# Optimization experiments

Measured on AMD Instinct MI355X. Metric: run time of the kernel, lower is better.

Reference implementation:

```python
import jax, jax.numpy as jnp
import numpy as np

B, C, H, W = 4, 256, 64, 64


def setup_inputs() -> dict:
    key = jax.random.key(0)
    ks = jax.random.split(key, 8)
    s = 0.02
    return {
        "x": jax.random.normal(ks[0], (B, C, H, W), dtype=jnp.float32),
        "Wq": jax.random.normal(ks[1], (C, C), dtype=jnp.float32) * s,
        "bq": jax.random.normal(ks[2], (C,), dtype=jnp.float32) * s,
        "Wk": jax.random.normal(ks[3], (C, C), dtype=jnp.float32) * s,
        "bk": jax.random.normal(ks[4], (C,), dtype=jnp.float32) * s,
        "Wv": jax.random.normal(ks[5], (C, C), dtype=jnp.float32) * s,
        "bv": jax.random.normal(ks[6], (C,), dtype=jnp.float32) * s,
        "gamma": jax.random.normal(ks[7], (1,), dtype=jnp.float32),
    }


def reference(x, Wq, bq, Wk, bk, Wv, bv, gamma):
    b, c, h, w = x.shape
    n = h * w
    xf = x.reshape(b, c, n)  # [B,C,N]
    # 1x1 convs == per-pixel linear over channels
    q = jnp.einsum("oc,bcn->bon", Wq, xf) + bq[None, :, None]  # [B,C,N]
    k = jnp.einsum("oc,bcn->bon", Wk, xf) + bk[None, :, None]  # [B,C,N]
    v = jnp.einsum("oc,bcn->bon", Wv, xf) + bv[None, :, None]  # [B,C,N]
    # energy[b,i,j] = sum_c q[b,c,i] * k[b,c,j]  (Q^T K, no scale in original)
    energy = jnp.einsum("bci,bcj->bij", q, k)  # [B,N,N]
    attention = jax.nn.softmax(energy, axis=-1)  # softmax over j
    # out = V @ attention^T : out[b,c,i] = sum_j v[b,c,j] * attention[b,i,j]
    out = jnp.einsum("bcj,bij->bci", v, attention)  # [B,C,N]
    out = gamma[0] * out + xf
    return out.reshape(b, c, h, w)
```

## Files before the change

kernel.cpp:

```cpp
#include <hip/hip_runtime.h>
#include <hip/hip_bf16.h>

#define Bb 4
#define Cc 256
#define Nn 4096
#define NV 4160

typedef short s16x8 __attribute__((ext_vector_type(8)));
typedef float f32x4 __attribute__((ext_vector_type(4)));

__device__ __forceinline__ unsigned short f2bf(float f) {
    unsigned u = __builtin_bit_cast(unsigned, f);
    u += 0x7FFFu + ((u >> 16) & 1u);
    return (unsigned short)(u >> 16);
}

__device__ __forceinline__ f32x4 mfma16(s16x8 a, s16x8 b, f32x4 c) {
    return __builtin_amdgcn_mfma_f32_16x16x32_bf16(a, b, c, 0, 0, 0);
}

#if __has_builtin(__builtin_amdgcn_global_load_lds)
#define GL16(g, sdst)                                                              \
    __builtin_amdgcn_global_load_lds(                                              \
        (const __attribute__((address_space(1))) unsigned int*)(g),                \
        (__attribute__((address_space(3))) unsigned int*)(sdst), 16, 0, 0)
#else
#define GL16(g, sdst)                                                              \
    do {                                                                           \
        *(s16x8*)((char*)(sdst) + (threadIdx.x & 63) * 16) = *(const s16x8*)(g);   \
    } while (0)
#endif

__global__ void prep_w(const float* __restrict__ Wq, const float* __restrict__ Wk,
                       const float* __restrict__ Wv, unsigned short* __restrict__ Wbf) {
    int idx = (blockIdx.x * 256 + threadIdx.x) * 8;
    int mat = idx >> 16;
    int off = idx & 65535;
    const float* src = (mat == 0) ? Wq : ((mat == 1) ? Wk : Wv);
    float4 a = *(const float4*)(src + off);
    float4 b = *(const float4*)(src + off + 4);
    s16x8 o;
    o[0] = (short)f2bf(a.x); o[1] = (short)f2bf(a.y);
    o[2] = (short)f2bf(a.z); o[3] = (short)f2bf(a.w);
    o[4] = (short)f2bf(b.x); o[5] = (short)f2bf(b.y);
    o[6] = (short)f2bf(b.z); o[7] = (short)f2bf(b.w);
    *(s16x8*)(Wbf + idx) = o;
}

__global__ void transpose_x(const float* __restrict__ x, unsigned short* __restrict__ xT) {
    int b = blockIdx.z, c0 = blockIdx.y * 64, n0 = blockIdx.x * 64;
    __shared__ float tile[64][65];
    int t = threadIdx.x;
    int r = t >> 2, q = t & 3;
    const float* src = x + ((size_t)(b * Cc + c0 + r)) * Nn + n0 + q * 16;
#pragma unroll
    for (int j = 0; j < 4; j++) {
        float4 v4 = *(const float4*)(src + j * 4);
        tile[r][q * 16 + j * 4 + 0] = v4.x;
        tile[r][q * 16 + j * 4 + 1] = v4.y;
        tile[r][q * 16 + j * 4 + 2] = v4.z;
        tile[r][q * 16 + j * 4 + 3] = v4.w;
    }
    __syncthreads();
    unsigned short* dst = xT + ((size_t)b * Nn + n0 + r) * Cc + c0 + q * 16;
    s16x8 o0, o1;
#pragma unroll
    for (int j = 0; j < 8; j++) o0[j] = (short)f2bf(tile[q * 16 + j][r]);
#pragma unroll
    for (int j = 0; j < 8; j++) o1[j] = (short)f2bf(tile[q * 16 + 8 + j][r]);
    *(s16x8*)dst = o0;
    *(s16x8*)(dst + 8) = o1;
}

__global__ void proj(const unsigned short* __restrict__ xT, const unsigned short* __restrict__ Wbf,
                     const float* __restrict__ bq, const float* __restrict__ bk,
                     const float* __restrict__ bv,
                     unsigned short* __restrict__ qT, unsigned short* __restrict__ kT,
                     unsigned short* __restrict__ vO) {
    int nt0 = blockIdx.x * 64;
    int mat = blockIdx.y;
    int b   = blockIdx.z;
    int t = threadIdx.x, w = t >> 6, l = t & 63;
    int lr = l & 15, lg = l >> 4;
    const unsigned short* Wm  = Wbf + mat * (Cc * Cc);
    const float* bias = (mat == 0) ? bq : ((mat == 1) ? bk : bv);
    const unsigned short* xTb = xT + (size_t)b * Nn * Cc;

    if (mat < 2) {
        unsigned short* out = ((mat == 0) ? qT : kT) + (size_t)b * Nn * Cc;
        int nrow = nt0 + w * 16;
        s16x8 af[8];
#pragma unroll
        for (int kk = 0; kk < 8; kk++)
            af[kk] = *(const s16x8*)(xTb + (nrow + lr) * Cc + kk * 32 + lg * 8);
        for (int ct = 0; ct < 16; ct++) {
            f32x4 acca = {0, 0, 0, 0}, accb = {0, 0, 0, 0};
#pragma unroll
            for (int kk = 0; kk < 8; kk += 2) {
                s16x8 bfa = *(const s16x8*)(Wm + (ct * 16 + lr) * Cc + kk * 32 + lg * 8);
                s16x8 bfb = *(const s16x8*)(Wm + (ct * 16 + lr) * Cc + (kk + 1) * 32 + lg * 8);
                acca = mfma16(af[kk], bfa, acca);
                accb = mfma16(af[kk + 1], bfb, accb);
            }
            f32x4 acc = acca + accb;
            float bb = bias[ct * 16 + lr];
#pragma unroll
            for (int r = 0; r < 4; r++)
                out[(nrow + lg * 4 + r) * Cc + ct * 16 + lr] = f2bf(acc[r] + bb);
        }
    } else {
        unsigned short* out = vO + (size_t)b * Cc * NV;
        for (int mt = 0; mt < 4; mt++) {
            int crow = (w * 4 + mt) * 16;
            s16x8 af[8];
#pragma unroll
            for (int kk = 0; kk < 8; kk++)
                af[kk] = *(const s16x8*)(Wm + (crow + lr) * Cc + kk * 32 + lg * 8);
#pragma unroll
            for (int nt = 0; nt < 4; nt++) {
                f32x4 acca = {0, 0, 0, 0}, accb = {0, 0, 0, 0};
#pragma unroll
                for (int kk = 0; kk < 8; kk += 2) {
                    s16x8 bfa = *(const s16x8*)(xTb + (nt0 + nt * 16 + lr) * Cc + kk * 32 + lg * 8);
                    s16x8 bfb = *(const s16x8*)(xTb + (nt0 + nt * 16 + lr) * Cc + (kk + 1) * 32 + lg * 8);
                    acca = mfma16(af[kk], bfa, acca);
                    accb = mfma16(af[kk + 1], bfb, accb);
                }
                f32x4 acc = acca + accb;
#pragma unroll
                for (int r = 0; r < 4; r++) {
                    float bb = bias[crow + lg * 4 + r];
                    out[(size_t)(crow + lg * 4 + r) * NV + nt0 + nt * 16 + lr] = f2bf(acc[r] + bb);
                }
            }
        }
    }
}

__global__ void __launch_bounds__(256, 2)
attn(const unsigned short* __restrict__ qT, const unsigned short* __restrict__ kT,
     const unsigned short* __restrict__ vv,
     float* __restrict__ OPT, float* __restrict__ lp) {
    int id = blockIdx.x;
    int bs = id & 7, b = bs >> 1, s = bs & 1, iblk = id >> 3;
    int t = threadIdx.x, w = t >> 6, l = t & 63;
    int lr = l & 15, lg = l >> 4;
    int i0 = iblk * 64 + w * 16;

    __shared__ char Ks[2][16384];
    __shared__ char Vs[2][16384];
    __shared__ unsigned short P_lds[4][512];
    unsigned short* pl = P_lds[w];

    const unsigned short* qb = qT + ((size_t)b * Nn + i0) * Cc;
    const char* kbase = (const char*)(kT + ((size_t)b * Nn + s * 2048) * Cc);
    const char* vbase = (const char*)(vv + (size_t)b * Cc * NV + s * 2048);

    s16x8 qf[8];
#pragma unroll
    for (int kk = 0; kk < 8; kk++)
        qf[kk] = *(const s16x8*)(qb + lr * Cc + kk * 32 + lg * 8);

    f32x4 O[16];
#pragma unroll
    for (int ct = 0; ct < 16; ct++) O[ct] = {0, 0, 0, 0};
    float lsum[4] = {0, 0, 0, 0};
    const float L2E = 1.44269504088896340736f;

#define STAGEK(bufi, jt)                                                        \
    {                                                                           \
        const char* ksl_ = kbase + (size_t)(jt) * 16384;                        \
        _Pragma("unroll") for (int i_ = 0; i_ < 4; i_++) {                      \
            int chunk_ = w * 4 + i_;                                            \
            int L_ = chunk_ * 1024 + l * 16;                                    \
            int row_ = L_ >> 9;                                                 \
            GL16(ksl_ + (L_ ^ ((row_ & 7) << 4)), &Ks[bufi][chunk_ * 1024]);    \
        }                                                                       \
    }

#define STAGEV(bufi, jt)                                                        \
    {                                                                           \
        _Pragma("unroll") for (int i_ = 0; i_ < 4; i_++) {                      \
            int chunk_ = w * 4 + i_;                                            \
            int row_ = chunk_ * 16 + (l >> 2);                                  \
            int colb_ = ((l & 3) * 16) ^ (((l >> 3) & 3) << 4);                 \
            GL16(vbase + (size_t)row_ * (NV * 2) + (size_t)(jt) * 64 + colb_,   \
                 &Vs[bufi][chunk_ * 1024]);                                     \
        }                                                                       \
    }

    STAGEK(0, 0);
    STAGEV(0, 0);
    asm volatile("s_waitcnt vmcnt(0)" ::: "memory");
    __syncthreads();
    int buf = 0;

    for (int jt = 0; jt < 64; jt++) {
        if (jt < 63) {
            STAGEK(buf ^ 1, jt + 1);
            STAGEV(buf ^ 1, jt + 1);
        }
        const char* ksb = Ks[buf];
        f32x4 E0 = {0, 0, 0, 0}, E1 = {0, 0, 0, 0};
#pragma unroll
        for (int kk = 0; kk < 8; kk++) {
            int cb = (kk * 64 + lg * 16) ^ ((lr & 7) << 4);
            s16x8 k0 = *(const s16x8*)(ksb + lr * 512 + cb);
            s16x8 k1 = *(const s16x8*)(ksb + (16 + lr) * 512 + cb);
            E0 = mfma16(qf[kk], k0, E0);
            E1 = mfma16(qf[kk], k1, E1);
        }
        float p0[4], p1[4];
#pragma unroll
        for (int r = 0; r < 4; r++) {
            p0[r] = exp2f(E0[r] * L2E);
            p1[r] = exp2f(E1[r] * L2E);
            lsum[r] += p0[r] + p1[r];
        }
#pragma unroll
        for (int r = 0; r < 4; r++) {
            pl[(lg * 4 + r) * 32 + lr] = f2bf(p0[r]);
            pl[(lg * 4 + r) * 32 + 16 + lr] = f2bf(p1[r]);
        }
        const char* vsb = Vs[buf];
        int vswz = (lg * 16) ^ (((lr >> 1) & 3) << 4);
        s16x8 vfr[16];
#pragma unroll
        for (int ct = 0; ct < 16; ct++)
            vfr[ct] = *(const s16x8*)(vsb + (ct * 16 + lr) * 64 + vswz);
        asm volatile("s_waitcnt lgkmcnt(0)" ::: "memory");
        __builtin_amdgcn_sched_barrier(0);
        s16x8 pf = *(const s16x8*)(pl + lr * 32 + lg * 8);
#pragma unroll
        for (int ct = 0; ct < 16; ct++)
            O[ct] = mfma16(pf, vfr[ct], O[ct]);
        asm volatile("s_waitcnt vmcnt(0)" ::: "memory");
        __syncthreads();
        buf ^= 1;
    }

#pragma unroll
    for (int r = 0; r < 4; r++) {
#pragma unroll
        for (int msk = 1; msk <= 8; msk <<= 1)
            lsum[r] += __shfl_xor(lsum[r], msk);
    }
    size_t sb = (size_t)(s * Bb + b);
    if (lr == 0) {
#pragma unroll
        for (int r = 0; r < 4; r++)
            lp[sb * Nn + i0 + lg * 4 + r] = lsum[r];
    }
    float* ob = OPT + sb * Nn * Cc;
#pragma unroll
    for (int ct = 0; ct < 16; ct++) {
#pragma unroll
        for (int r = 0; r < 4; r++)
            ob[(size_t)(i0 + lg * 4 + r) * Cc + ct * 16 + lr] = O[ct][r];
    }
#undef STAGEK
#undef STAGEV
}

__global__ void __launch_bounds__(256)
merge(const float* __restrict__ OPT, const float* __restrict__ lp,
      const float* __restrict__ x, const float* __restrict__ gamma,
      float* __restrict__ out) {
    int b = blockIdx.z, c0 = blockIdx.y * 64, n0 = blockIdx.x * 64;
    __shared__ float tile[64][65];
    __shared__ float linv[64];
    int t = threadIdx.x;
    if (t < 64) {
        float sum = lp[(size_t)b * Nn + n0 + t] + lp[(size_t)(Bb + b) * Nn + n0 + t];
        linv[t] = 1.0f / sum;
    }
    __syncthreads();
    float g = gamma[0];
    int r = t >> 2, q = t & 3;
    const float* p0 = OPT + ((size_t)b * Nn + n0 + r) * Cc + c0 + q * 16;
    const float* p1 = OPT + ((size_t)(Bb + b) * Nn + n0 + r) * Cc + c0 + q * 16;
    float sc = g * linv[r];
#pragma unroll
    for (int j = 0; j < 4; j++) {
        float4 a0 = *(const float4*)(p0 + j * 4);
        float4 a1 = *(const float4*)(p1 + j * 4);
        tile[r][q * 16 + j * 4 + 0] = sc * (a0.x + a1.x);
        tile[r][q * 16 + j * 4 + 1] = sc * (a0.y + a1.y);
        tile[r][q * 16 + j * 4 + 2] = sc * (a0.z + a1.z);
        tile[r][q * 16 + j * 4 + 3] = sc * (a0.w + a1.w);
    }
    __syncthreads();
    const float* xp = x + ((size_t)b * Cc + c0 + r) * Nn + n0 + q * 16;
    float* op = out + ((size_t)b * Cc + c0 + r) * Nn + n0 + q * 16;
#pragma unroll
    for (int j = 0; j < 4; j++) {
        float4 xv = *(const float4*)(xp + j * 4);
        float4 o4;
        o4.x = tile[q * 16 + j * 4 + 0][r] + xv.x;
        o4.y = tile[q * 16 + j * 4 + 1][r] + xv.y;
        o4.z = tile[q * 16 + j * 4 + 2][r] + xv.z;
        o4.w = tile[q * 16 + j * 4 + 3][r] + xv.w;
        *(float4*)(op + j * 4) = o4;
    }
}

extern "C" void kernel_launch(void* const* d_in, const int* in_sizes, int n_in,
                              void* d_out, int out_size, void* d_ws, size_t ws_size,
                              hipStream_t stream) {
    (void)in_sizes; (void)n_in; (void)out_size; (void)ws_size;
    const float* x     = (const float*)d_in[0];
    const float* Wq    = (const float*)d_in[1];
    const float* bq    = (const float*)d_in[2];
    const float* Wk    = (const float*)d_in[3];
    const float* bk    = (const float*)d_in[4];
    const float* Wv    = (const float*)d_in[5];
    const float* bv    = (const float*)d_in[6];
    const float* gamma = (const float*)d_in[7];
    float* out = (float*)d_out;

    const size_t XTN = (size_t)Bb * Nn * Cc;
    const size_t VSZ = (size_t)Bb * Cc * NV;
    unsigned short* xT  = (unsigned short*)d_ws;
    unsigned short* Wbf = xT + XTN;
    unsigned short* qT  = Wbf + 3 * Cc * Cc;
    unsigned short* kT  = qT + XTN;
    unsigned short* vv  = kT + XTN;
    float*          OPT = (float*)(vv + VSZ);
    float*          lp  = OPT + 2 * XTN;

    hipLaunchKernelGGL(prep_w, dim3(96), dim3(256), 0, stream, Wq, Wk, Wv, Wbf);
    hipLaunchKernelGGL(transpose_x, dim3(Nn / 64, Cc / 64, Bb), dim3(256), 0, stream, x, xT);
    hipLaunchKernelGGL(proj, dim3(Nn / 64, 3, Bb), dim3(256), 0, stream,
                       xT, Wbf, bq, bk, bv, qT, kT, vv);
    hipLaunchKernelGGL(attn, dim3(512), dim3(256), 0, stream,
                       qT, kT, vv, OPT, lp);
    hipLaunchKernelGGL(merge, dim3(Nn / 64, Cc / 64, Bb), dim3(256), 0, stream,
                       OPT, lp, x, gamma, out);
}
```

Measured before the change: 180.1 us.

## Transpose MFMA operands and shuffle P in registers instead of LDS round-trip

```diff
diff --git a/kernel.cpp b/kernel.cpp
--- a/kernel.cpp
+++ b/kernel.cpp
@@ -13,6 +13,10 @@
     unsigned u = __builtin_bit_cast(unsigned, f);
     u += 0x7FFFu + ((u >> 16) & 1u);
     return (unsigned short)(u >> 16);
+}
+
+__device__ __forceinline__ unsigned pk2bf(float a, float b) {
+    return (unsigned)f2bf(a) | ((unsigned)f2bf(b) << 16);
 }
 
 __device__ __forceinline__ f32x4 mfma16(s16x8 a, s16x8 b, f32x4 c) {
@@ -149,8 +153,6 @@
 
     __shared__ char Ks[2][16384];
     __shared__ char Vs[2][16384];
-    __shared__ unsigned short P_lds[4][512];
-    unsigned short* pl = P_lds[w];
 
     const unsigned short* qb = qT + ((size_t)b * Nn + i0) * Cc;
     const char* kbase = (const char*)(kT + ((size_t)b * Nn + s * 2048) * Cc);
@@ -164,7 +166,7 @@
     f32x4 O[16];
 #pragma unroll
     for (int ct = 0; ct < 16; ct++) O[ct] = {0, 0, 0, 0};
-    float lsum[4] = {0, 0, 0, 0};
+    float lsum = 0.f;
     const float L2E = 1.44269504088896340736f;
 
 #define STAGEK(bufi, jt)                                                        \
@@ -202,62 +204,67 @@
         }
         const char* ksb = Ks[buf];
         f32x4 E0 = {0, 0, 0, 0}, E1 = {0, 0, 0, 0};
+        __builtin_amdgcn_s_setprio(1);
 #pragma unroll
         for (int kk = 0; kk < 8; kk++) {
             int cb = (kk * 64 + lg * 16) ^ ((lr & 7) << 4);
             s16x8 k0 = *(const s16x8*)(ksb + lr * 512 + cb);
             s16x8 k1 = *(const s16x8*)(ksb + (16 + lr) * 512 + cb);
-            E0 = mfma16(qf[kk], k0, E0);
-            E1 = mfma16(qf[kk], k1, E1);
-        }
+            E0 = mfma16(k0, qf[kk], E0);
+            E1 = mfma16(k1, qf[kk], E1);
+        }
+        __builtin_amdgcn_s_setprio(0);
+        const char* vsb = Vs[buf];
+        int vswz = (lg * 16) ^ (((lr >> 1) & 3) << 4);
+        s16x8 vfr[16];
+#pragma unroll
+        for (int ct = 0; ct < 16; ct++)
+            vfr[ct] = *(const s16x8*)(vsb + (ct * 16 + lr) * 64 + vswz);
         float p0[4], p1[4];
 #pragma unroll
         for (int r = 0; r < 4; r++) {
             p0[r] = exp2f(E0[r] * L2E);
             p1[r] = exp2f(E1[r] * L2E);
-            lsum[r] += p0[r] + p1[r];
-        }
-#pragma unroll
-        for (int r = 0; r < 4; r++) {
-            pl[(lg * 4 + r) * 32 + lr] = f2bf(p0[r]);
-            pl[(lg * 4 + r) * 32 + 16 + lr] = f2bf(p1[r]);
-        }
-        const char* vsb = Vs[buf];
-        int vswz = (lg * 16) ^ (((lr >> 1) & 3) << 4);
-        s16x8 vfr[16];
+            lsum += p0[r] + p1[r];
+        }
+        unsigned h0a = pk2bf(p0[0], p0[1]), h0b = pk2bf(p0[2], p0[3]);
+        unsigned h1a = pk2bf(p1[0], p1[1]), h1b = pk2bf(p1[2], p1[3]);
+        int sA = lr + ((lg & 1) << 5);
+        int sB = sA + 16;
+        unsigned a0 = (unsigned)__shfl((int)h0a, sA);
+        unsigned b0 = (unsigned)__shfl((int)h1a, sA);
+        unsigned a1 = (unsigned)__shfl((int)h0b, sA);
+        unsigned b1 = (unsigned)__shfl((int)h1b, sA);
+        unsigned a2 = (unsigned)__shfl((int)h0a, sB);
+        unsigned b2 = (unsigned)__shfl((int)h1a, sB);
+        unsigned a3 = (unsigned)__shfl((int)h0b, sB);
+        unsigned b3 = (unsigned)__shfl((int)h1b, sB);
+        bool losel = (lg < 2);
+        uint4 pw;
+        pw.x = losel ? a0 : b0;
+        pw.y = losel ? a1 : b1;
+        pw.z = losel ? a2 : b2;
+        pw.w = losel ? a3 : b3;
+        s16x8 pf = __builtin_bit_cast(s16x8, pw);
+        __builtin_amdgcn_s_setprio(1);
 #pragma unroll
         for (int ct = 0; ct < 16; ct++)
-            vfr[ct] = *(const s16x8*)(vsb + (ct * 16 + lr) * 64 + vswz);
-        asm volatile("s_waitcnt lgkmcnt(0)" ::: "memory");
-        __builtin_amdgcn_sched_barrier(0);
-        s16x8 pf = *(const s16x8*)(pl + lr * 32 + lg * 8);
-#pragma unroll
-        for (int ct = 0; ct < 16; ct++)
-            O[ct] = mfma16(pf, vfr[ct], O[ct]);
+            O[ct] = mfma16(vfr[ct], pf, O[ct]);
+        __builtin_amdgcn_s_setprio(0);
         asm volatile("s_waitcnt vmcnt(0)" ::: "memory");
         __syncthreads();
         buf ^= 1;
     }
 
-#pragma unroll
-    for (int r = 0; r < 4; r++) {
-#pragma unroll
-        for (int msk = 1; msk <= 8; msk <<= 1)
-            lsum[r] += __shfl_xor(lsum[r], msk);
-    }
+    lsum += __shfl_xor(lsum, 16);
+    lsum += __shfl_xor(lsum, 32);
     size_t sb = (size_t)(s * Bb + b);
-    if (lr == 0) {
-#pragma unroll
-        for (int r = 0; r < 4; r++)
-            lp[sb * Nn + i0 + lg * 4 + r] = lsum[r];
-    }
+    if (lg == 0)
+        lp[sb * Nn + i0 + lr] = lsum;
     float* ob = OPT + sb * Nn * Cc;
 #pragma unroll
-    for (int ct = 0; ct < 16; ct++) {
-#pragma unroll
-        for (int r = 0; r < 4; r++)
-            ob[(size_t)(i0 + lg * 4 + r) * Cc + ct * 16 + lr] = O[ct][r];
-    }
+    for (int ct = 0; ct < 16; ct++)
+        *(f32x4*)(ob + (size_t)(i0 + lr) * Cc + ct * 16 + lg * 4) = O[ct];
 #undef STAGEK
 #undef STAGEV
 }
```

Result: slower. 186.5 us (+3.5%).

## Use 32x32 MFMA in attention with register P, 4-way key split, bf16 partials

Applied to the files above, without the earlier changes.

```diff
diff --git a/kernel.cpp b/kernel.cpp
--- a/kernel.cpp
+++ b/kernel.cpp
@@ -8,15 +8,26 @@
 
 typedef short s16x8 __attribute__((ext_vector_type(8)));
 typedef float f32x4 __attribute__((ext_vector_type(4)));
+typedef float f32x16 __attribute__((ext_vector_type(16)));
 
 __device__ __forceinline__ unsigned short f2bf(float f) {
     unsigned u = __builtin_bit_cast(unsigned, f);
     u += 0x7FFFu + ((u >> 16) & 1u);
     return (unsigned short)(u >> 16);
 }
+__device__ __forceinline__ float bf2f(unsigned short u) {
+    unsigned v = ((unsigned)u) << 16;
+    return __builtin_bit_cast(float, v);
+}
+__device__ __forceinline__ unsigned pk2bf(float a, float b) {
+    return (unsigned)f2bf(a) | ((unsigned)f2bf(b) << 16);
+}
 
 __device__ __forceinline__ f32x4 mfma16(s16x8 a, s16x8 b, f32x4 c) {
     return __builtin_amdgcn_mfma_f32_16x16x32_bf16(a, b, c, 0, 0, 0);
+}
+__device__ __forceinline__ f32x16 mfma32(s16x8 a, s16x8 b, f32x16 c) {
+    return __builtin_amdgcn_mfma_f32_32x32x16_bf16(a, b, c, 0, 0, 0);
 }
 
 #if __has_builtin(__builtin_amdgcn_global_load_lds)
@@ -140,31 +151,34 @@
 __global__ void __launch_bounds__(256, 2)
 attn(const unsigned short* __restrict__ qT, const unsigned short* __restrict__ kT,
      const unsigned short* __restrict__ vv,
-     float* __restrict__ OPT, float* __restrict__ lp) {
+     unsigned short* __restrict__ OPT, float* __restrict__ lp) {
     int id = blockIdx.x;
-    int bs = id & 7, b = bs >> 1, s = bs & 1, iblk = id >> 3;
+    int xcd = id & 7, k = id >> 3;
+    int combo = xcd * 2 + (k & 1);
+    int b = combo >> 2, s = combo & 3;
+    int iblk = k >> 1;
     int t = threadIdx.x, w = t >> 6, l = t & 63;
-    int lr = l & 15, lg = l >> 4;
-    int i0 = iblk * 64 + w * 16;
+    int la = l & 31, lh = l >> 5;
+    int i0 = iblk * 128 + w * 32;
 
     __shared__ char Ks[2][16384];
     __shared__ char Vs[2][16384];
-    __shared__ unsigned short P_lds[4][512];
-    unsigned short* pl = P_lds[w];
 
     const unsigned short* qb = qT + ((size_t)b * Nn + i0) * Cc;
-    const char* kbase = (const char*)(kT + ((size_t)b * Nn + s * 2048) * Cc);
-    const char* vbase = (const char*)(vv + (size_t)b * Cc * NV + s * 2048);
-
-    s16x8 qf[8];
-#pragma unroll
-    for (int kk = 0; kk < 8; kk++)
-        qf[kk] = *(const s16x8*)(qb + lr * Cc + kk * 32 + lg * 8);
-
-    f32x4 O[16];
-#pragma unroll
-    for (int ct = 0; ct < 16; ct++) O[ct] = {0, 0, 0, 0};
-    float lsum[4] = {0, 0, 0, 0};
+    const char* kbase = (const char*)(kT + ((size_t)b * Nn + s * 1024) * Cc);
+    const char* vbase = (const char*)(vv + (size_t)b * Cc * NV + s * 1024);
+
+    s16x8 qf[16];
+#pragma unroll
+    for (int kk = 0; kk < 16; kk++)
+        qf[kk] = *(const s16x8*)(qb + la * Cc + kk * 16 + lh * 8);
+
+    f32x16 O[8];
+#pragma unroll
+    for (int ct = 0; ct < 8; ct++)
+#pragma unroll
+        for (int r = 0; r < 16; r++) O[ct][r] = 0.f;
+    float lsum = 0.f;
     const float L2E = 1.44269504088896340736f;
 
 #define STAGEK(bufi, jt)                                                        \
@@ -195,112 +209,129 @@
     __syncthreads();
     int buf = 0;
 
-    for (int jt = 0; jt < 64; jt++) {
-        if (jt < 63) {
+    for (int jt = 0; jt < 32; jt++) {
+        if (jt < 31) {
             STAGEK(buf ^ 1, jt + 1);
             STAGEV(buf ^ 1, jt + 1);
         }
         const char* ksb = Ks[buf];
-        f32x4 E0 = {0, 0, 0, 0}, E1 = {0, 0, 0, 0};
-#pragma unroll
-        for (int kk = 0; kk < 8; kk++) {
-            int cb = (kk * 64 + lg * 16) ^ ((lr & 7) << 4);
-            s16x8 k0 = *(const s16x8*)(ksb + lr * 512 + cb);
-            s16x8 k1 = *(const s16x8*)(ksb + (16 + lr) * 512 + cb);
-            E0 = mfma16(qf[kk], k0, E0);
-            E1 = mfma16(qf[kk], k1, E1);
-        }
-        float p0[4], p1[4];
-#pragma unroll
-        for (int r = 0; r < 4; r++) {
-            p0[r] = exp2f(E0[r] * L2E);
-            p1[r] = exp2f(E1[r] * L2E);
-            lsum[r] += p0[r] + p1[r];
-        }
-#pragma unroll
-        for (int r = 0; r < 4; r++) {
-            pl[(lg * 4 + r) * 32 + lr] = f2bf(p0[r]);
-            pl[(lg * 4 + r) * 32 + 16 + lr] = f2bf(p1[r]);
-        }
+        f32x16 E;
+#pragma unroll
+        for (int r = 0; r < 16; r++) E[r] = 0.f;
+        __builtin_amdgcn_s_setprio(1);
+#pragma unroll
+        for (int kk = 0; kk < 16; kk++) {
+            s16x8 kf = *(const s16x8*)(ksb + la * 512 +
+                                       ((kk * 32 + lh * 16) ^ ((l & 7) << 4)));
+            E = mfma32(kf, qf[kk], E);
+        }
+        __builtin_amdgcn_s_setprio(0);
+#pragma unroll
+        for (int r = 0; r < 16; r++) {
+            float pv = exp2f(E[r] * L2E);
+            E[r] = pv;
+            lsum += pv;
+        }
+        unsigned pk0 = pk2bf(E[0], E[1]),   pk1 = pk2bf(E[2], E[3]);
+        unsigned pk2 = pk2bf(E[4], E[5]),   pk3 = pk2bf(E[6], E[7]);
+        unsigned pk4 = pk2bf(E[8], E[9]),   pk5 = pk2bf(E[10], E[11]);
+        unsigned pk6 = pk2bf(E[12], E[13]), pk7 = pk2bf(E[14], E[15]);
+        unsigned x0 = (unsigned)__shfl_xor((int)pk0, 32);
+        unsigned x1 = (unsigned)__shfl_xor((int)pk1, 32);
+        unsigned x2 = (unsigned)__shfl_xor((int)pk2, 32);
+        unsigned x3 = (unsigned)__shfl_xor((int)pk3, 32);
+        unsigned x4 = (unsigned)__shfl_xor((int)pk4, 32);
+        unsigned x5 = (unsigned)__shfl_xor((int)pk5, 32);
+        unsigned x6 = (unsigned)__shfl_xor((int)pk6, 32);
+        unsigned x7 = (unsigned)__shfl_xor((int)pk7, 32);
+        bool h1 = (lh == 1);
+        uint4 w0, w1;
+        w0.x = h1 ? x2 : pk0;  w0.y = h1 ? x3 : pk1;
+        w0.z = h1 ? pk2 : x0;  w0.w = h1 ? pk3 : x1;
+        w1.x = h1 ? x6 : pk4;  w1.y = h1 ? x7 : pk5;
+        w1.z = h1 ? pk6 : x4;  w1.w = h1 ? pk7 : x5;
+        s16x8 pf0 = __builtin_bit_cast(s16x8, w0);
+        s16x8 pf1 = __builtin_bit_cast(s16x8, w1);
         const char* vsb = Vs[buf];
-        int vswz = (lg * 16) ^ (((lr >> 1) & 3) << 4);
-        s16x8 vfr[16];
-#pragma unroll
-        for (int ct = 0; ct < 16; ct++)
-            vfr[ct] = *(const s16x8*)(vsb + (ct * 16 + lr) * 64 + vswz);
-        asm volatile("s_waitcnt lgkmcnt(0)" ::: "memory");
-        __builtin_amdgcn_sched_barrier(0);
-        s16x8 pf = *(const s16x8*)(pl + lr * 32 + lg * 8);
-#pragma unroll
-        for (int ct = 0; ct < 16; ct++)
-            O[ct] = mfma16(pf, vfr[ct], O[ct]);
+        int vsw = ((l >> 1) & 3) << 4;
+        __builtin_amdgcn_s_setprio(1);
+#pragma unroll
+        for (int ct = 0; ct < 8; ct++) {
+            s16x8 va = *(const s16x8*)(vsb + (ct * 32 + la) * 64 +
+                                       ((lh * 16) ^ vsw));
+            O[ct] = mfma32(va, pf0, O[ct]);
+            s16x8 vb = *(const s16x8*)(vsb + (ct * 32 + la) * 64 +
+                                       ((32 + lh * 16) ^ vsw));
+            O[ct] = mfma32(vb, pf1, O[ct]);
+        }
+        __builtin_amdgcn_s_setprio(0);
         asm volatile("s_waitcnt vmcnt(0)" ::: "memory");
         __syncthreads();
         buf ^= 1;
     }
 
-#pragma unroll
-    for (int r = 0; r < 4; r++) {
-#pragma unroll
-        for (int msk = 1; msk <= 8; msk <<= 1)
-            lsum[r] += __shfl_xor(lsum[r], msk);
-    }
-    size_t sb = (size_t)(s * Bb + b);
-    if (lr == 0) {
-#pragma unroll
-        for (int r = 0; r < 4; r++)
-            lp[sb * Nn + i0 + lg * 4 + r] = lsum[r];
-    }
-    float* ob = OPT + sb * Nn * Cc;
-#pragma unroll
-    for (int ct = 0; ct < 16; ct++) {
-#pragma unroll
-        for (int r = 0; r < 4; r++)
-            ob[(size_t)(i0 + lg * 4 + r) * Cc + ct * 16 + lr] = O[ct][r];
+    lsum += __shfl_xor(lsum, 32);
+    if (l < 32)
+        lp[(size_t)combo * Nn + i0 + l] = lsum;
+    unsigned short* ob = OPT + (size_t)combo * Cc * Nn;
+#pragma unroll
+    for (int ct = 0; ct < 8; ct++) {
+#pragma unroll
+        for (int g = 0; g < 4; g++) {
+#pragma unroll
+            for (int r = 0; r < 4; r++) {
+                int c = ct * 32 + 8 * g + 4 * lh + r;
+                ob[(size_t)c * Nn + i0 + la] = f2bf(O[ct][4 * g + r]);
+            }
+        }
     }
 #undef STAGEK
 #undef STAGEV
 }
 
 __global__ void __launch_bounds__(256)
-merge(const float* __restrict__ OPT, const float* __restrict__ lp,
+merge(const unsigned short* __restrict__ OPT, const float* __restrict__ lp,
       const float* __restrict__ x, const float* __restrict__ gamma,
       float* __restrict__ out) {
     int b = blockIdx.z, c0 = blockIdx.y * 64, n0 = blockIdx.x * 64;
-    __shared__ float tile[64][65];
     __shared__ float linv[64];
     int t = threadIdx.x;
     if (t < 64) {
-        float sum = lp[(size_t)b * Nn + n0 + t] + lp[(size_t)(Bb + b) * Nn + n0 + t];
+        float sum = 0.f;
+#pragma unroll
+        for (int si = 0; si < 4; si++)
+            sum += lp[(size_t)(b * 4 + si) * Nn + n0 + t];
         linv[t] = 1.0f / sum;
     }
     __syncthreads();
     float g = gamma[0];
     int r = t >> 2, q = t & 3;
-    const float* p0 = OPT + ((size_t)b * Nn + n0 + r) * Cc + c0 + q * 16;
-    const float* p1 = OPT + ((size_t)(Bb + b) * Nn + n0 + r) * Cc + c0 + q * 16;
-    float sc = g * linv[r];
-#pragma unroll
-    for (int j = 0; j < 4; j++) {
-        float4 a0 = *(const float4*)(p0 + j * 4);
-        float4 a1 = *(const float4*)(p1 + j * 4);
-        tile[r][q * 16 + j * 4 + 0] = sc * (a0.x + a1.x);
-        tile[r][q * 16 + j * 4 + 1] = sc * (a0.y + a1.y);
-        tile[r][q * 16 + j * 4 + 2] = sc * (a0.z + a1.z);
-        tile[r][q * 16 + j * 4 + 3] = sc * (a0.w + a1.w);
-    }
-    __syncthreads();
-    const float* xp = x + ((size_t)b * Cc + c0 + r) * Nn + n0 + q * 16;
-    float* op = out + ((size_t)b * Cc + c0 + r) * Nn + n0 + q * 16;
-#pragma unroll
-    for (int j = 0; j < 4; j++) {
-        float4 xv = *(const float4*)(xp + j * 4);
+    int c = c0 + r;
+    float acc[16];
+#pragma unroll
+    for (int j = 0; j < 16; j++) acc[j] = 0.f;
+#pragma unroll
+    for (int si = 0; si < 4; si++) {
+        const unsigned short* p = OPT + ((size_t)((b * 4 + si) * Cc + c)) * Nn + n0 + q * 16;
+        s16x8 v0 = *(const s16x8*)p;
+        s16x8 v1 = *(const s16x8*)(p + 8);
+#pragma unroll
+        for (int j = 0; j < 8; j++) {
+            acc[j] += bf2f((unsigned short)v0[j]);
+            acc[8 + j] += bf2f((unsigned short)v1[j]);
+        }
+    }
+    const float* xp = x + ((size_t)b * Cc + c) * Nn + n0 + q * 16;
+    float* op = out + ((size_t)b * Cc + c) * Nn + n0 + q * 16;
+#pragma unroll
+    for (int j4 = 0; j4 < 4; j4++) {
+        float4 xv = *(const float4*)(xp + j4 * 4);
         float4 o4;
-        o4.x = tile[q * 16 + j * 4 + 0][r] + xv.x;
-        o4.y = tile[q * 16 + j * 4 + 1][r] + xv.y;
-        o4.z = tile[q * 16 + j * 4 + 2][r] + xv.z;
-        o4.w = tile[q * 16 + j * 4 + 3][r] + xv.w;
-        *(float4*)(op + j * 4) = o4;
+        o4.x = g * acc[j4 * 4 + 0] * linv[q * 16 + j4 * 4 + 0] + xv.x;
+        o4.y = g * acc[j4 * 4 + 1] * linv[q * 16 + j4 * 4 + 1] + xv.y;
+        o4.z = g * acc[j4 * 4 + 2] * linv[q * 16 + j4 * 4 + 2] + xv.z;
+        o4.w = g * acc[j4 * 4 + 3] * linv[q * 16 + j4 * 4 + 3] + xv.w;
+        *(float4*)(op + j4 * 4) = o4;
     }
 }
 
@@ -325,8 +356,8 @@
     unsigned short* qT  = Wbf + 3 * Cc * Cc;
     unsigned short* kT  = qT + XTN;
     unsigned short* vv  = kT + XTN;
-    float*          OPT = (float*)(vv + VSZ);
-    float*          lp  = OPT + 2 * XTN;
+    unsigned short* OPT = vv + VSZ;
+    float*          lp  = (float*)(OPT + (size_t)16 * Nn * Cc);
 
     hipLaunchKernelGGL(prep_w, dim3(96), dim3(256), 0, stream, Wq, Wk, Wv, Wbf);
     hipLaunchKernelGGL(transpose_x, dim3(Nn / 64, Cc / 64, Bb), dim3(256), 0, stream, x, xT);
```

After: 183.7 us. 2.0% more time.
